# Kernel tuning notes

Hardware: AMD Instinct MI355X
Metric: run time of the kernel (lower is better)

Reference implementation:

```python
import jax, jax.numpy as jnp
import numpy as np

H = W = 32      # latent grid
WS = 8          # window size
NH = 8          # heads
C = 512         # channels
SHIFTS = (0, WS // 2)  # depth-2 Swin stage: W-MSA then SW-MSA


def _rel_pos_index(ws):
    coords = np.stack(np.meshgrid(np.arange(ws), np.arange(ws), indexing='ij'))
    flat = coords.reshape(2, -1)
    rel = (flat[:, :, None] - flat[:, None, :]).transpose(1, 2, 0).copy()
    rel[:, :, 0] += ws - 1
    rel[:, :, 1] += ws - 1
    rel[:, :, 0] *= 2 * ws - 1
    return jnp.asarray(rel.sum(-1))  # (ws*ws, ws*ws) int


def _attn_mask(h, w, ws, shift):
    img = np.zeros((h, w))
    cnt = 0
    sl = (slice(0, -ws), slice(-ws, -shift), slice(-shift, None))
    for hs in sl:
        for wsl in sl:
            img[hs, wsl] = cnt
            cnt += 1
    mw = img.reshape(h // ws, ws, w // ws, ws).transpose(0, 2, 1, 3).reshape(-1, ws * ws)
    m = mw[:, None, :] - mw[:, :, None]  # matches unsqueeze(1) - unsqueeze(2)
    return jnp.asarray(np.where(m != 0, -100.0, 0.0).astype(np.float32))  # (nW, N, N)


def _ln(x, g, b, eps=1e-5):
    mu = x.mean(-1, keepdims=True)
    var = ((x - mu) ** 2).mean(-1, keepdims=True)
    return (x - mu) * jax.lax.rsqrt(var + eps) * g + b


def _swin_block(x, shift, mask, rpi, n1g, n1b, qw, qb, rpb, pw, pb, n2g, n2b, f1w, f1b, f2w, f2b):
    B, L, Cc = x.shape
    N = WS * WS
    hd = Cc // NH
    shortcut = x
    h = _ln(x, n1g, n1b).reshape(B, H, W, Cc)
    if shift > 0:
        h = jnp.roll(h, (-shift, -shift), (1, 2))
    # window partition -> (B*nW, N, C)
    hw = h.reshape(B, H // WS, WS, W // WS, WS, Cc).transpose(0, 1, 3, 2, 4, 5).reshape(-1, N, Cc)
    qkv = (hw @ qw + qb).reshape(-1, N, 3, NH, hd).transpose(2, 0, 3, 1, 4)
    q, k, v = qkv[0], qkv[1], qkv[2]
    attn = jnp.einsum('bhnd,bhmd->bhnm', q * (hd ** -0.5), k)
    bias = rpb[rpi.reshape(-1)].reshape(N, N, NH).transpose(2, 0, 1)  # (NH, N, N)
    attn = attn + bias[None]
    if mask is not None:
        nW = mask.shape[0]
        attn = attn.reshape(-1, nW, NH, N, N) + mask[None, :, None]
        attn = attn.reshape(-1, NH, N, N)
    attn = jax.nn.softmax(attn, axis=-1)
    o = jnp.einsum('bhnm,bhmd->bhnd', attn, v).transpose(0, 2, 1, 3).reshape(-1, N, Cc)
    o = o @ pw + pb
    # window reverse
    o = o.reshape(B, H // WS, W // WS, WS, WS, Cc).transpose(0, 1, 3, 2, 4, 5).reshape(B, H, W, Cc)
    if shift > 0:
        o = jnp.roll(o, (shift, shift), (1, 2))
    x = shortcut + o.reshape(B, L, Cc)
    h2 = _ln(x, n2g, n2b)
    x = x + (jax.nn.gelu(h2 @ f1w + f1b, approximate=False) @ f2w + f2b)
    return x


def setup_inputs() -> dict:
    key = jax.random.key(0)
    ks = jax.random.split(key, 8)
    B, D, K = 32, 2, 4096
    s = 0.02
    return {
        'x': jax.random.normal(ks[0], (B, H * W, C), jnp.float32),
        'norm1_g': jnp.ones((D, C), jnp.float32),
        'norm1_b': jnp.zeros((D, C), jnp.float32),
        'qkv_w': jax.random.normal(ks[1], (D, C, 3 * C), jnp.float32) * s,
        'qkv_b': jnp.zeros((D, 3 * C), jnp.float32),
        'rpb_table': jax.random.normal(ks[2], (D, (2 * WS - 1) ** 2, NH), jnp.float32) * s,
        'proj_w': jax.random.normal(ks[3], (D, C, C), jnp.float32) * s,
        'proj_b': jnp.zeros((D, C), jnp.float32),
        'norm2_g': jnp.ones((D, C), jnp.float32),
        'norm2_b': jnp.zeros((D, C), jnp.float32),
        'fc1_w': jax.random.normal(ks[4], (D, C, 4 * C), jnp.float32) * s,
        'fc1_b': jnp.zeros((D, 4 * C), jnp.float32),
        'fc2_w': jax.random.normal(ks[5], (D, 4 * C, C), jnp.float32) * s,
        'fc2_b': jnp.zeros((D, C), jnp.float32),
        'codebook': jax.random.normal(ks[6], (K, C), jnp.float32),
    }


def reference(x, norm1_g, norm1_b, qkv_w, qkv_b, rpb_table, proj_w, proj_b,
              norm2_g, norm2_b, fc1_w, fc1_b, fc2_w, fc2_b, codebook):
    B, L, Cc = x.shape
    rpi = _rel_pos_index(WS)
    masks = [None, _attn_mask(H, W, WS, SHIFTS[1])]
    for i, shift in enumerate(SHIFTS):
        x = _swin_block(x, shift, masks[i], rpi,
                        norm1_g[i], norm1_b[i], qkv_w[i], qkv_b[i], rpb_table[i],
                        proj_w[i], proj_b[i], norm2_g[i], norm2_b[i],
                        fc1_w[i], fc1_b[i], fc2_w[i], fc2_b[i])
    # nearest-neighbor codebook quantization (cdist + argmin + gather)
    flat = x.reshape(-1, Cc)
    d = ((flat ** 2).sum(-1, keepdims=True)
         - 2.0 * flat @ codebook.T
         + (codebook ** 2).sum(-1))  # (B*L, K)
    idx = jnp.argmin(d, axis=-1)
    quant = codebook[idx]
    # straight-through estimator
    quant = flat + jax.lax.stop_gradient(quant - flat)
    return quant.reshape(B, L, Cc), idx.reshape(B, L)
```

## Files before the change

kernel.cpp:

```cpp
#include <hip/hip_runtime.h>
#include <math.h>

#define DEV __device__ __forceinline__

typedef __attribute__((ext_vector_type(8))) _Float16 f16x8;
typedef __attribute__((ext_vector_type(8))) short short8;
typedef __attribute__((ext_vector_type(4))) float f32x4;

namespace {

constexpr int C = 512;
constexpr int ROWS = 32768;
constexpr float LSCALE = 2048.0f;
constexpr float LINV   = 1.0f / 2048.0f;
constexpr float F16MIN = 6.1035156e-5f;

DEV void f2hsplit(float x, short& hs, short& ls) {
  _Float16 h = (_Float16)x;
  float hf = (float)h;
  if (fabsf(hf) < F16MIN) { h = (_Float16)0.0f; hf = 0.f; }
  _Float16 l = (_Float16)((x - hf) * LSCALE);
  if (fabsf((float)l) < F16MIN) l = (_Float16)0.0f;
  hs = __builtin_bit_cast(short, h);
  ls = __builtin_bit_cast(short, l);
}

DEV unsigned umn(unsigned a, unsigned b) { return a < b ? a : b; }
DEV unsigned umx(unsigned a, unsigned b) { return a > b ? a : b; }

DEV unsigned packkey(float d, int col) {
  unsigned u = __builtin_bit_cast(unsigned, d);
  u = (u & 0x80000000u) ? ~u : (u | 0x80000000u);
  return (u & 0xFFFFF000u) | (unsigned)col;
}
DEV float unpackd(unsigned k) {
  unsigned u = (k & 0x80000000u) ? (k ^ 0x80000000u) : ~k;
  return __builtin_bit_cast(float, u);
}

DEV int rowmap(int r, int shift) {
  int b  = r >> 10;
  int w  = (r >> 6) & 15;
  int wy = w >> 2, wx = w & 3;
  int ii = r & 63;
  int iy = ii >> 3, ix = ii & 7;
  int y = (wy * 8 + iy + shift) & 31;
  int x = (wx * 8 + ix + shift) & 31;
  return (b << 10) + (y << 5) + x;
}

DEV int region(int y) { return (y < 24) ? 0 : ((y < 28) ? 1 : 2); }

typedef __attribute__((address_space(1))) const unsigned int gu32;
typedef __attribute__((address_space(3))) unsigned int lu32;
DEV void gload16(const void* g, void* l) {
  __builtin_amdgcn_global_load_lds((gu32*)g, (lu32*)l, 16, 0, 0);
}

__global__ __launch_bounds__(256) void ln_split_kernel(
    const float* __restrict__ src, short* __restrict__ Hp, short* __restrict__ Lp,
    const float* __restrict__ g, const float* __restrict__ b,
    int shift, int windowed) {
  int wid  = (blockIdx.x * 256 + threadIdx.x) >> 6;
  int lane = threadIdx.x & 63;
  if (wid >= ROWS) return;
  int srcRow = windowed ? rowmap(wid, shift) : wid;
  const float* s = src + (size_t)srcRow * C + lane * 8;
  float v[8];
  *(float4*)(v)     = *(const float4*)(s);
  *(float4*)(v + 4) = *(const float4*)(s + 4);
  float sum = 0.f;
#pragma unroll
  for (int j = 0; j < 8; j++) sum += v[j];
#pragma unroll
  for (int o = 32; o >= 1; o >>= 1) sum += __shfl_xor(sum, o);
  float mu = sum * (1.0f / 512.0f);
  float vs = 0.f;
#pragma unroll
  for (int j = 0; j < 8; j++) { float d = v[j] - mu; vs += d * d; }
#pragma unroll
  for (int o = 32; o >= 1; o >>= 1) vs += __shfl_xor(vs, o);
  float rs = rsqrtf(vs * (1.0f / 512.0f) + 1e-5f);
  float gg[8], bb[8];
  *(float4*)gg       = *(const float4*)&g[lane * 8];
  *(float4*)(gg + 4) = *(const float4*)&g[lane * 8 + 4];
  *(float4*)bb       = *(const float4*)&b[lane * 8];
  *(float4*)(bb + 4) = *(const float4*)&b[lane * 8 + 4];
  short8 hv, lv;
#pragma unroll
  for (int j = 0; j < 8; j++) {
    float o8 = (v[j] - mu) * rs * gg[j] + bb[j];
    short hh, ll;
    f2hsplit(o8, hh, ll);
    hv[j] = hh; lv[j] = ll;
  }
  *(short8*)&Hp[(size_t)wid * C + lane * 8] = hv;
  *(short8*)&Lp[(size_t)wid * C + lane * 8] = lv;
}

__global__ __launch_bounds__(256) void rowss_kernel(
    const float* __restrict__ src, float* __restrict__ dst, int nrows) {
  int wid  = (blockIdx.x * 256 + threadIdx.x) >> 6;
  int lane = threadIdx.x & 63;
  if (wid >= nrows) return;
  const float* s = src + (size_t)wid * C + lane * 8;
  float4 a  = *(const float4*)s;
  float4 b4 = *(const float4*)(s + 4);
  float sum = a.x*a.x + a.y*a.y + a.z*a.z + a.w*a.w
            + b4.x*b4.x + b4.y*b4.y + b4.z*b4.z + b4.w*b4.w;
#pragma unroll
  for (int o = 32; o >= 1; o >>= 1) sum += __shfl_xor(sum, o);
  if (lane == 0) dst[wid] = sum;
}

__global__ __launch_bounds__(256) void wconvT_kernel(
    const float* __restrict__ W, short* __restrict__ Hp, short* __restrict__ Lp,
    int K, int N) {
  __shared__ float t[32][33];
  int tx = threadIdx.x, ty = threadIdx.y;
  int n0 = blockIdx.x * 32, k0 = blockIdx.y * 32;
#pragma unroll
  for (int r = 0; r < 4; r++) {
    int k = ty + r * 8;
    t[k][tx] = W[(size_t)(k0 + k) * N + n0 + tx];
  }
  __syncthreads();
#pragma unroll
  for (int r = 0; r < 4; r++) {
    int n = ty + r * 8;
    short h, l;
    f2hsplit(t[tx][n], h, l);
    Hp[(size_t)(n0 + n) * K + k0 + tx] = h;
    Lp[(size_t)(n0 + n) * K + k0 + tx] = l;
  }
}

__global__ __launch_bounds__(256) void wconv_kernel(
    const float* __restrict__ W, short* __restrict__ Hp, short* __restrict__ Lp) {
  size_t i = ((size_t)blockIdx.x * 256 + threadIdx.x) * 4;
  float4 a = *(const float4*)&W[i];
  float v[4] = {a.x, a.y, a.z, a.w};
  short hv[4], lv[4];
#pragma unroll
  for (int j = 0; j < 4; j++) f2hsplit(v[j], hv[j], lv[j]);
  *(short4*)&Hp[i] = *(short4*)hv;
  *(short4*)&Lp[i] = *(short4*)lv;
}

template <int EPI>
__global__ __launch_bounds__(512) void mgemm(
    const short* __restrict__ Ah, const short* __restrict__ Al,
    const short* __restrict__ Bh, const short* __restrict__ Bl,
    const int K, const float* __restrict__ bias,
    float* __restrict__ outF, short* __restrict__ outH, short* __restrict__ outL,
    const int ldo,
    const float* __restrict__ resid, const int rowOff, const int perm, const int shift) {
  __shared__ short lds[16384];
  const int m0 = blockIdx.x * 128, n0 = blockIdx.y * 128;
  const int t  = threadIdx.x;
  const int wv = t >> 6, ln = t & 63;
  const int wr = (wv >> 2) * 64, wc = (wv & 3) * 32;
  const int l15 = ln & 15, l4 = ln >> 4;

  f32x4 accH[4][2], accL[4][2];
#pragma unroll
  for (int mf = 0; mf < 4; mf++)
#pragma unroll
    for (int nf = 0; nf < 2; nf++) {
      accH[mf][nf] = (f32x4){0.f, 0.f, 0.f, 0.f};
      accL[mf][nf] = (f32x4){0.f, 0.f, 0.f, 0.f};
    }

  const int srow = ln >> 2;
  const int scol = ((ln & 3) ^ ((ln >> 3) & 3)) * 8;

  short* As_h = lds;
  short* Bs_h = lds + 4096;
  short* As_l = lds + 8192;
  short* Bs_l = lds + 12288;

  auto frag = [&](const short* lt, int rbase) -> f16x8 {
    int r = rbase + l15;
    int kc = l4 ^ ((r >> 1) & 3);
    return *(const f16x8*)(lt + (r >> 4) * 512 + (r & 15) * 32 + kc * 8);
  };

  for (int k0 = 0; k0 < K; k0 += 32) {
    size_t ra = (size_t)(m0 + wv * 16 + srow) * K + k0 + scol;
    size_t rb = (size_t)(n0 + wv * 16 + srow) * K + k0 + scol;
    gload16(Ah + ra, As_h + wv * 512);
    gload16(Bh + rb, Bs_h + wv * 512);
    gload16(Al + ra, As_l + wv * 512);
    gload16(Bl + rb, Bs_l + wv * 512);
    __syncthreads();
    f16x8 ah[4], bh[2], bl[2];
#pragma unroll
    for (int mf = 0; mf < 4; mf++) ah[mf] = frag(As_h, wr + mf * 16);
#pragma unroll
    for (int nf = 0; nf < 2; nf++) bh[nf] = frag(Bs_h, wc + nf * 16);
#pragma unroll
    for (int mf = 0; mf < 4; mf++)
#pragma unroll
      for (int nf = 0; nf < 2; nf++)
        accH[mf][nf] = __builtin_amdgcn_mfma_f32_16x16x32_f16(ah[mf], bh[nf], accH[mf][nf], 0, 0, 0);
#pragma unroll
    for (int nf = 0; nf < 2; nf++) bl[nf] = frag(Bs_l, wc + nf * 16);
#pragma unroll
    for (int mf = 0; mf < 4; mf++)
#pragma unroll
      for (int nf = 0; nf < 2; nf++)
        accL[mf][nf] = __builtin_amdgcn_mfma_f32_16x16x32_f16(ah[mf], bl[nf], accL[mf][nf], 0, 0, 0);
#pragma unroll
    for (int mf = 0; mf < 4; mf++) {
      f16x8 al = frag(As_l, wr + mf * 16);
#pragma unroll
      for (int nf = 0; nf < 2; nf++)
        accL[mf][nf] = __builtin_amdgcn_mfma_f32_16x16x32_f16(al, bh[nf], accL[mf][nf], 0, 0, 0);
    }
    __syncthreads();
  }

  f32x4 acc[4][2];
#pragma unroll
  for (int mf = 0; mf < 4; mf++)
#pragma unroll
    for (int nf = 0; nf < 2; nf++)
#pragma unroll
      for (int r = 0; r < 4; r++)
        acc[mf][nf][r] = fmaf(accL[mf][nf][r], LINV, accH[mf][nf][r]);

  if (EPI == 0) {
#pragma unroll
    for (int mf = 0; mf < 4; mf++)
#pragma unroll
      for (int r = 0; r < 4; r++) {
        int row = m0 + wr + mf * 16 + l4 * 4 + r;
        float* op = outF + (size_t)row * ldo;
#pragma unroll
        for (int nf = 0; nf < 2; nf++) {
          int col = n0 + wc + nf * 16 + l15;
          op[col] = acc[mf][nf][r] + bias[col];
        }
      }
  } else if (EPI == 1) {
#pragma unroll
    for (int mf = 0; mf < 4; mf++)
#pragma unroll
      for (int r = 0; r < 4; r++) {
        int row = m0 + wr + mf * 16 + l4 * 4 + r;
#pragma unroll
        for (int nf = 0; nf < 2; nf++) {
          int col = n0 + wc + nf * 16 + l15;
          float v = acc[mf][nf][r] + bias[col];
          v = 0.5f * v * (1.0f + erff(v * 0.70710678118654752f));
          short h, l;
          f2hsplit(v, h, l);
          outH[(size_t)row * ldo + col] = h;
          outL[(size_t)row * ldo + col] = l;
        }
      }
  } else {
#pragma unroll
    for (int mf = 0; mf < 4; mf++)
#pragma unroll
      for (int r = 0; r < 4; r++) {
        int row = m0 + wr + mf * 16 + l4 * 4 + r;
        int orow = perm ? rowmap(row, shift) : (row + rowOff);
        const float* rp = resid + (size_t)orow * ldo;
        float* op = outF + (size_t)orow * ldo;
#pragma unroll
        for (int nf = 0; nf < 2; nf++) {
          int col = n0 + wc + nf * 16 + l15;
          float v = rp[col] + acc[mf][nf][r] + bias[col];
          op[col] = v;
          if (EPI == 4) {
            short h, l;
            f2hsplit(v, h, l);
            outH[(size_t)orow * ldo + col] = h;
            outL[(size_t)orow * ldo + col] = l;
          }
        }
      }
  }
}

__global__ __launch_bounds__(256) void vqgemm(
    const short* __restrict__ Ah, const short* __restrict__ Bh,
    const float* __restrict__ c2, unsigned* __restrict__ pk) {
  __shared__ short lds[16384];
  const int bid = blockIdx.x;
  const int xcd = bid & 7, idx = bid >> 3;
  const int m0 = (xcd * 32 + (idx & 31)) * 128;
  const int ny = idx >> 5;
  const int n0 = ny * 128;
  const int K = 512;
  const int t  = threadIdx.x;
  const int wv = t >> 6, ln = t & 63;
  const int wr = (wv >> 1) * 64, wc = (wv & 1) * 64;
  const int l15 = ln & 15, l4 = ln >> 4;

  f32x4 acc[4][4];
#pragma unroll
  for (int mf = 0; mf < 4; mf++)
#pragma unroll
    for (int nf = 0; nf < 4; nf++) acc[mf][nf] = (f32x4){0.f, 0.f, 0.f, 0.f};

  const int srow = ln >> 2;
  const int scol = ((ln & 3) ^ ((ln >> 3) & 3)) * 8;

  short* As = lds;
  short* Bs = lds + 8192;

  auto frag = [&](const short* lt, int rbase) -> f16x8 {
    int r = rbase + l15;
    int kc = l4 ^ ((r >> 1) & 3);
    return *(const f16x8*)(lt + (r >> 4) * 512 + (r & 15) * 32 + kc * 8);
  };

  for (int k0 = 0; k0 < K; k0 += 64) {
#pragma unroll
    for (int q = 0; q < 8; q++) {
      int s = wv * 8 + q;
      int c = s & 15;
      int base0 = (s < 16) ? m0 : n0;
      const short* src = (s < 16) ? Ah : Bh;
      short* dst = ((s < 16) ? As : Bs) + c * 512;
      size_t ga = (size_t)(base0 + (c & 7) * 16 + srow) * K + k0 + (c >> 3) * 32 + scol;
      gload16(src + ga, dst);
    }
    __syncthreads();
#pragma unroll
    for (int kh = 0; kh < 2; kh++) {
      const short* Ab = As + kh * 4096;
      const short* Bb = Bs + kh * 4096;
      f16x8 ah[4], bh[4];
#pragma unroll
      for (int mf = 0; mf < 4; mf++) ah[mf] = frag(Ab, wr + mf * 16);
#pragma unroll
      for (int nf = 0; nf < 4; nf++) bh[nf] = frag(Bb, wc + nf * 16);
#pragma unroll
      for (int mf = 0; mf < 4; mf++)
#pragma unroll
        for (int nf = 0; nf < 4; nf++)
          acc[mf][nf] = __builtin_amdgcn_mfma_f32_16x16x32_f16(ah[mf], bh[nf], acc[mf][nf], 0, 0, 0);
    }
    __syncthreads();
  }

  unsigned* hk = (unsigned*)(void*)lds;
#pragma unroll
  for (int mf = 0; mf < 4; mf++)
#pragma unroll
    for (int r = 0; r < 4; r++) {
      int wrow = wr + mf * 16 + l4 * 4 + r;
      unsigned k1 = 0xFFFFFFFFu, k2 = 0xFFFFFFFFu;
#pragma unroll
      for (int nf = 0; nf < 4; nf++) {
        int col = n0 + wc + nf * 16 + l15;
        float d = c2[col] - 2.0f * acc[mf][nf][r];
        unsigned kk = packkey(d, col);
        if (kk < k1) { k2 = k1; k1 = kk; }
        else if (kk < k2) { k2 = kk; }
      }
#pragma unroll
      for (int o = 1; o <= 8; o <<= 1) {
        unsigned b1 = (unsigned)__shfl_xor((int)k1, o);
        unsigned b2 = (unsigned)__shfl_xor((int)k2, o);
        unsigned m1 = umn(k1, b1);
        unsigned m2 = umn(umx(k1, b1), umn(k2, b2));
        k1 = m1; k2 = m2;
      }
      if (l15 == 0) {
        hk[wrow * 4 + (wv & 1) * 2 + 0] = k1;
        hk[wrow * 4 + (wv & 1) * 2 + 1] = k2;
      }
    }
  __syncthreads();
  if (t < 128) {
    unsigned a1 = hk[t * 4 + 0], a2 = hk[t * 4 + 1];
    unsigned b1 = hk[t * 4 + 2], b2 = hk[t * 4 + 3];
    unsigned m1 = umn(a1, b1);
    unsigned m2 = umn(umx(a1, b1), umn(a2, b2));
    size_t base = (size_t)(m0 + t) * 64 + ny * 2;
    pk[base + 0] = m1;
    pk[base + 1] = m2;
  }
}

__global__ __launch_bounds__(256) void vq_out_kernel(
    const unsigned* __restrict__ pk, const float* __restrict__ x,
    const float* __restrict__ cb,
    float* __restrict__ outq, float* __restrict__ outidx) {
  int r = blockIdx.x * 4 + (threadIdx.x >> 6);
  int lane = threadIdx.x & 63;
  unsigned key = pk[(size_t)r * 64 + lane];
  unsigned kmin = key;
#pragma unroll
  for (int o = 32; o >= 1; o >>= 1) kmin = umn(kmin, (unsigned)__shfl_xor((int)kmin, o));
  float dmin = unpackd(kmin);
  unsigned long long mask = __ballot(unpackd(key) <= dmin + 2.0f);

  const float* xr = x + (size_t)r * C + lane * 8;
  float4 xa = *(const float4*)xr;
  float4 xb = *(const float4*)(xr + 4);

  float bestd = 3.4e38f;
  int   besti = 0x7fffffff;
  while (mask) {
    int l = __ffsll(mask) - 1;
    mask &= mask - 1;
    int col = ((unsigned)__shfl((int)key, l)) & 0xFFFu;
    const float* cr = cb + (size_t)col * C + lane * 8;
    float4 ca = *(const float4*)cr;
    float4 cb4 = *(const float4*)(cr + 4);
    float s = 0.f;
    s = fmaf(ca.x, ca.x - 2.f * xa.x, s);
    s = fmaf(ca.y, ca.y - 2.f * xa.y, s);
    s = fmaf(ca.z, ca.z - 2.f * xa.z, s);
    s = fmaf(ca.w, ca.w - 2.f * xa.w, s);
    s = fmaf(cb4.x, cb4.x - 2.f * xb.x, s);
    s = fmaf(cb4.y, cb4.y - 2.f * xb.y, s);
    s = fmaf(cb4.z, cb4.z - 2.f * xb.z, s);
    s = fmaf(cb4.w, cb4.w - 2.f * xb.w, s);
#pragma unroll
    for (int o = 32; o >= 1; o >>= 1) s += __shfl_xor(s, o);
    if (s < bestd || (s == bestd && col < besti)) { bestd = s; besti = col; }
  }
  const float4* src = (const float4*)(cb + (size_t)besti * C + lane * 8);
  float4*       dst = (float4*)(outq + (size_t)r * C + lane * 8);
  dst[0] = src[0];
  dst[1] = src[1];
  if (lane == 0) outidx[r] = (float)besti;
}

__global__ __launch_bounds__(256) void attn_kernel(
    const float* __restrict__ qkv,
    const float* __restrict__ rpb,
    short* __restrict__ Hout, short* __restrict__ Lout,
    int winOff, int shift) {
  int wl = blockIdx.x;
  int h  = blockIdx.y;
  int t  = threadIdx.x;
  __shared__ float q[64][64], k[64][64], v[64][64], pT[64][64];

  const float* base = qkv + (size_t)wl * 64 * 1536 + h * 64;
#pragma unroll
  for (int rep = 0; rep < 4; rep++) {
    int f = t + rep * 256;
    int i = f >> 4, dq = (f & 15) * 4;
    const float* rowp = base + (size_t)i * 1536 + dq;
    float4 qv = *(const float4*)(rowp);
    float4 kv = *(const float4*)(rowp + 512);
    float4 vv = *(const float4*)(rowp + 1024);
    q[i][dq] = qv.x * 0.125f; q[i][dq + 1] = qv.y * 0.125f;
    q[i][dq + 2] = qv.z * 0.125f; q[i][dq + 3] = qv.w * 0.125f;
    *(float4*)&k[i][dq] = kv;
    *(float4*)&v[i][dq] = vv;
  }
  __syncthreads();

  int i  = t >> 2;
  int jg = t & 3;
  int wim = (winOff + wl) & 15;
  int wy = wim >> 2, wx = wim & 3;
  int iy = i >> 3, ix = i & 7;

  float qreg[64];
#pragma unroll
  for (int d = 0; d < 64; d += 4) *(float4*)&qreg[d] = *(float4*)&q[i][d];

  int ci = 0;
  if (shift) ci = region(wy * 8 + iy) * 3 + region(wx * 8 + ix);

  float sc[16];
#pragma unroll
  for (int jj = 0; jj < 16; jj++) {
    int j = jg * 16 + jj;
    float s = 0.f;
#pragma unroll
    for (int d = 0; d < 64; d += 4) {
      float4 kv = *(float4*)&k[j][d];
      s = fmaf(qreg[d], kv.x, s);
      s = fmaf(qreg[d + 1], kv.y, s);
      s = fmaf(qreg[d + 2], kv.z, s);
      s = fmaf(qreg[d + 3], kv.w, s);
    }
    int jy = j >> 3, jx = j & 7;
    s += rpb[((iy - jy + 7) * 15 + (ix - jx + 7)) * 8 + h];
    if (shift) {
      int cj = region(wy * 8 + jy) * 3 + region(wx * 8 + jx);
      if (ci != cj) s -= 100.0f;
    }
    sc[jj] = s;
  }
  float mx = sc[0];
#pragma unroll
  for (int jj = 1; jj < 16; jj++) mx = fmaxf(mx, sc[jj]);
  mx = fmaxf(mx, __shfl_xor(mx, 1));
  mx = fmaxf(mx, __shfl_xor(mx, 2));
  float sum = 0.f;
#pragma unroll
  for (int jj = 0; jj < 16; jj++) { sc[jj] = expf(sc[jj] - mx); sum += sc[jj]; }
  sum += __shfl_xor(sum, 1);
  sum += __shfl_xor(sum, 2);
  float inv = 1.0f / sum;
#pragma unroll
  for (int jj = 0; jj < 16; jj++) pT[jg * 16 + jj][i] = sc[jj] * inv;
  __syncthreads();

  float accv[16];
#pragma unroll
  for (int dd = 0; dd < 16; dd++) accv[dd] = 0.f;
  for (int j = 0; j < 64; j++) {
    float pij = pT[j][i];
#pragma unroll
    for (int dd = 0; dd < 16; dd += 4) {
      float4 vv = *(float4*)&v[j][jg * 16 + dd];
      accv[dd]     = fmaf(pij, vv.x, accv[dd]);
      accv[dd + 1] = fmaf(pij, vv.y, accv[dd + 1]);
      accv[dd + 2] = fmaf(pij, vv.z, accv[dd + 2]);
      accv[dd + 3] = fmaf(pij, vv.w, accv[dd + 3]);
    }
  }
  size_t obase = ((size_t)(winOff + wl) * 64 + i) * 512 + h * 64 + jg * 16;
  short8 hv, lv;
#pragma unroll
  for (int half = 0; half < 2; half++) {
#pragma unroll
    for (int j = 0; j < 8; j++) {
      short hh, ll;
      f2hsplit(accv[half * 8 + j], hh, ll);
      hv[j] = hh; lv[j] = ll;
    }
    *(short8*)&Hout[obase + half * 8] = hv;
    *(short8*)&Lout[obase + half * 8] = lv;
  }
}

}

extern "C" void kernel_launch(void* const* d_in, const int* in_sizes, int n_in,
                              void* d_out, int out_size, void* d_ws, size_t ws_size,
                              hipStream_t stream) {
  const float* x_in = (const float*)d_in[0];
  const float* n1g  = (const float*)d_in[1];
  const float* n1b  = (const float*)d_in[2];
  const float* qkvw = (const float*)d_in[3];
  const float* qkvb = (const float*)d_in[4];
  const float* rpb  = (const float*)d_in[5];
  const float* pw   = (const float*)d_in[6];
  const float* pb   = (const float*)d_in[7];
  const float* n2g  = (const float*)d_in[8];
  const float* n2b  = (const float*)d_in[9];
  const float* f1w  = (const float*)d_in[10];
  const float* f1b  = (const float*)d_in[11];
  const float* f2w  = (const float*)d_in[12];
  const float* f2b_ = (const float*)d_in[13];
  const float* cb   = (const float*)d_in[14];

  float* outq   = (float*)d_out;
  float* outidx = outq + 16777216;
  short* Hbuf = (short*)d_out;
  short* Lbuf = Hbuf + (size_t)ROWS * 512;

  char* ws = (char*)d_ws;
  float* Abuf = (float*)ws;
  short* Wb   = (short*)(ws + ((size_t)64 << 20));
  char*  Cbuf = ws + ((size_t)96 << 20);
  const int Rrows = (ws_size >= ((size_t)232 << 20)) ? 16384
                  : (ws_size >= ((size_t)160 << 20)) ? 8192
                  : (ws_size >= ((size_t)128 << 20)) ? 4096 : 2048;

  const int SZ_QKV = 512 * 1536, SZ_P = 512 * 512, SZ_F1 = 512 * 2048, SZ_F2 = 2048 * 512;
  const int PB = (SZ_QKV + SZ_P + SZ_F1 + SZ_F2) * 2;
  short* cbH = Wb + (size_t)2 * PB;
  short* cbL = cbH + 4096 * 512;

  for (int blk = 0; blk < 2; blk++) {
    short* base = Wb + (size_t)blk * PB;
    short* qH = base;          short* qL = qH + SZ_QKV;
    short* pH = qL + SZ_QKV;   short* pL = pH + SZ_P;
    short* f1H = pL + SZ_P;    short* f1L = f1H + SZ_F1;
    short* f2H = f1L + SZ_F1;  short* f2L = f2H + SZ_F2;
    wconvT_kernel<<<dim3(48, 16), dim3(32, 8), 0, stream>>>(qkvw + (size_t)blk * SZ_QKV, qH, qL, 512, 1536);
    wconvT_kernel<<<dim3(16, 16), dim3(32, 8), 0, stream>>>(pw + (size_t)blk * SZ_P, pH, pL, 512, 512);
    wconvT_kernel<<<dim3(64, 16), dim3(32, 8), 0, stream>>>(f1w + (size_t)blk * SZ_F1, f1H, f1L, 512, 2048);
    wconvT_kernel<<<dim3(16, 64), dim3(32, 8), 0, stream>>>(f2w + (size_t)blk * SZ_F2, f2H, f2L, 2048, 512);
  }
  wconv_kernel<<<2048, 256, 0, stream>>>(cb, cbH, cbL);

  const int nch = ROWS / Rrows;
  for (int blk = 0; blk < 2; blk++) {
    short* base = Wb + (size_t)blk * PB;
    short* qH = base;          short* qL = qH + SZ_QKV;
    short* pH = qL + SZ_QKV;   short* pL = pH + SZ_P;
    short* f1H = pL + SZ_P;    short* f1L = f1H + SZ_F1;
    short* f2H = f1L + SZ_F1;  short* f2L = f2H + SZ_F2;
    const float* xcur = blk ? (const float*)Abuf : x_in;
    int shift = blk ? 4 : 0;

    ln_split_kernel<<<8192, 256, 0, stream>>>(xcur, Hbuf, Lbuf, n1g + blk * 512, n1b + blk * 512, shift, 1);

    float* Cq = (float*)Cbuf;
    for (int ch = 0; ch < nch; ch++) {
      int r0 = ch * Rrows;
      mgemm<0><<<dim3(Rrows / 128, 12), 512, 0, stream>>>(
          Hbuf + (size_t)r0 * 512, Lbuf + (size_t)r0 * 512, qH, qL, 512,
          qkvb + blk * 1536, Cq, nullptr, nullptr, 1536,
          nullptr, 0, 0, 0);
      attn_kernel<<<dim3(Rrows / 64, 8), 256, 0, stream>>>(
          Cq, rpb + blk * 1800, Hbuf, Lbuf, r0 >> 6, shift);
    }

    mgemm<2><<<dim3(256, 4), 512, 0, stream>>>(
        Hbuf, Lbuf, pH, pL, 512, pb + blk * 512,
        Abuf, nullptr, nullptr, 512,
        blk ? (const float*)Abuf : x_in, 0, 1, shift);

    ln_split_kernel<<<8192, 256, 0, stream>>>(Abuf, Hbuf, Lbuf, n2g + blk * 512, n2b + blk * 512, 0, 0);

    short* gh = (short*)Cbuf;
    short* gl = gh + (size_t)Rrows * 2048;
    for (int ch = 0; ch < nch; ch++) {
      int r0 = ch * Rrows;
      mgemm<1><<<dim3(Rrows / 128, 16), 512, 0, stream>>>(
          Hbuf + (size_t)r0 * 512, Lbuf + (size_t)r0 * 512, f1H, f1L, 512,
          f1b + blk * 2048, nullptr, gh, gl, 2048,
          nullptr, 0, 0, 0);
      if (blk == 0) {
        mgemm<2><<<dim3(Rrows / 128, 4), 512, 0, stream>>>(
            gh, gl, f2H, f2L, 2048, f2b_ + blk * 512,
            Abuf, nullptr, nullptr, 512,
            Abuf, r0, 0, 0);
      } else {
        mgemm<4><<<dim3(Rrows / 128, 4), 512, 0, stream>>>(
            gh, gl, f2H, f2L, 2048, f2b_ + blk * 512,
            Abuf, Hbuf, Lbuf, 512,
            Abuf, r0, 0, 0);
      }
    }
  }

  float*    c2  = (float*)Cbuf;
  unsigned* pkb = (unsigned*)(Cbuf + ((size_t)64 << 10));
  rowss_kernel<<<1024, 256, 0, stream>>>(cb, c2, 4096);
  vqgemm<<<8192, 256, 0, stream>>>(Hbuf, cbH, c2, pkb);
  vq_out_kernel<<<8192, 256, 0, stream>>>(pkb, Abuf, cb, outq, outidx);
}
```

Measured before the change: 2.424 ms.

## Double-buffer LDS in split-f16 GEMM and restructure VQ GEMM to 512 threads

The mgemm kernel now keeps two LDS buffers and issues the global-to-LDS loads for the next K slice before computing the current one, so memory latency can overlap with MFMA work. This doubles its shared-memory footprint and may lower occupancy. The vqgemm kernel moves to 512 threads with 8 waves, each computing a 64x32 sub-tile. It steps K by 32 with the same double-buffered staging, and its top-2 reduction now merges four partial results per row instead of two.

```diff
diff --git a/kernel.cpp b/kernel.cpp
--- a/kernel.cpp
+++ b/kernel.cpp
@@ -155,7 +155,7 @@
     float* __restrict__ outF, short* __restrict__ outH, short* __restrict__ outL,
     const int ldo,
     const float* __restrict__ resid, const int rowOff, const int perm, const int shift) {
-  __shared__ short lds[16384];
+  __shared__ short lds[32768];
   const int m0 = blockIdx.x * 128, n0 = blockIdx.y * 128;
   const int t  = threadIdx.x;
   const int wv = t >> 6, ln = t & 63;
@@ -174,25 +174,31 @@
   const int srow = ln >> 2;
   const int scol = ((ln & 3) ^ ((ln >> 3) & 3)) * 8;
 
-  short* As_h = lds;
-  short* Bs_h = lds + 4096;
-  short* As_l = lds + 8192;
-  short* Bs_l = lds + 12288;
-
+  auto stage = [&](int buf, int k0) {
+    short* b = lds + buf * 16384;
+    size_t ra = (size_t)(m0 + wv * 16 + srow) * K + k0 + scol;
+    size_t rb = (size_t)(n0 + wv * 16 + srow) * K + k0 + scol;
+    gload16(Ah + ra, b + wv * 512);
+    gload16(Bh + rb, b + 4096 + wv * 512);
+    gload16(Al + ra, b + 8192 + wv * 512);
+    gload16(Bl + rb, b + 12288 + wv * 512);
+  };
   auto frag = [&](const short* lt, int rbase) -> f16x8 {
     int r = rbase + l15;
     int kc = l4 ^ ((r >> 1) & 3);
     return *(const f16x8*)(lt + (r >> 4) * 512 + (r & 15) * 32 + kc * 8);
   };
 
+  stage(0, 0);
+  __syncthreads();
+  int cur = 0;
   for (int k0 = 0; k0 < K; k0 += 32) {
-    size_t ra = (size_t)(m0 + wv * 16 + srow) * K + k0 + scol;
-    size_t rb = (size_t)(n0 + wv * 16 + srow) * K + k0 + scol;
-    gload16(Ah + ra, As_h + wv * 512);
-    gload16(Bh + rb, Bs_h + wv * 512);
-    gload16(Al + ra, As_l + wv * 512);
-    gload16(Bl + rb, Bs_l + wv * 512);
-    __syncthreads();
+    if (k0 + 32 < K) stage(cur ^ 1, k0 + 32);
+    const short* base = lds + cur * 16384;
+    const short* As_h = base;
+    const short* Bs_h = base + 4096;
+    const short* As_l = base + 8192;
+    const short* Bs_l = base + 12288;
     f16x8 ah[4], bh[2], bl[2];
 #pragma unroll
     for (int mf = 0; mf < 4; mf++) ah[mf] = frag(As_h, wr + mf * 16);
@@ -218,6 +224,7 @@
         accL[mf][nf] = __builtin_amdgcn_mfma_f32_16x16x32_f16(al, bh[nf], accL[mf][nf], 0, 0, 0);
     }
     __syncthreads();
+    cur ^= 1;
   }
 
   f32x4 acc[4][2];
@@ -284,7 +291,7 @@
   }
 }
 
-__global__ __launch_bounds__(256) void vqgemm(
+__global__ __launch_bounds__(512) void vqgemm(
     const short* __restrict__ Ah, const short* __restrict__ Bh,
     const float* __restrict__ c2, unsigned* __restrict__ pk) {
   __shared__ short lds[16384];
@@ -296,55 +303,49 @@
   const int K = 512;
   const int t  = threadIdx.x;
   const int wv = t >> 6, ln = t & 63;
-  const int wr = (wv >> 1) * 64, wc = (wv & 1) * 64;
+  const int wr = (wv >> 2) * 64, wc = (wv & 3) * 32;
   const int l15 = ln & 15, l4 = ln >> 4;
 
-  f32x4 acc[4][4];
+  f32x4 acc[4][2];
 #pragma unroll
   for (int mf = 0; mf < 4; mf++)
 #pragma unroll
-    for (int nf = 0; nf < 4; nf++) acc[mf][nf] = (f32x4){0.f, 0.f, 0.f, 0.f};
+    for (int nf = 0; nf < 2; nf++) acc[mf][nf] = (f32x4){0.f, 0.f, 0.f, 0.f};
 
   const int srow = ln >> 2;
   const int scol = ((ln & 3) ^ ((ln >> 3) & 3)) * 8;
 
-  short* As = lds;
-  short* Bs = lds + 8192;
-
+  auto stage = [&](int buf, int k0) {
+    short* b = lds + buf * 8192;
+    size_t ra = (size_t)(m0 + wv * 16 + srow) * K + k0 + scol;
+    size_t rb = (size_t)(n0 + wv * 16 + srow) * K + k0 + scol;
+    gload16(Ah + ra, b + wv * 512);
+    gload16(Bh + rb, b + 4096 + wv * 512);
+  };
   auto frag = [&](const short* lt, int rbase) -> f16x8 {
     int r = rbase + l15;
     int kc = l4 ^ ((r >> 1) & 3);
     return *(const f16x8*)(lt + (r >> 4) * 512 + (r & 15) * 32 + kc * 8);
   };
 
-  for (int k0 = 0; k0 < K; k0 += 64) {
-#pragma unroll
-    for (int q = 0; q < 8; q++) {
-      int s = wv * 8 + q;
-      int c = s & 15;
-      int base0 = (s < 16) ? m0 : n0;
-      const short* src = (s < 16) ? Ah : Bh;
-      short* dst = ((s < 16) ? As : Bs) + c * 512;
-      size_t ga = (size_t)(base0 + (c & 7) * 16 + srow) * K + k0 + (c >> 3) * 32 + scol;
-      gload16(src + ga, dst);
-    }
+  stage(0, 0);
+  __syncthreads();
+  int cur = 0;
+  for (int k0 = 0; k0 < K; k0 += 32) {
+    if (k0 + 32 < K) stage(cur ^ 1, k0 + 32);
+    const short* base = lds + cur * 8192;
+    f16x8 ah[4], bh[2];
+#pragma unroll
+    for (int mf = 0; mf < 4; mf++) ah[mf] = frag(base, wr + mf * 16);
+#pragma unroll
+    for (int nf = 0; nf < 2; nf++) bh[nf] = frag(base + 4096, wc + nf * 16);
+#pragma unroll
+    for (int mf = 0; mf < 4; mf++)
+#pragma unroll
+      for (int nf = 0; nf < 2; nf++)
+        acc[mf][nf] = __builtin_amdgcn_mfma_f32_16x16x32_f16(ah[mf], bh[nf], acc[mf][nf], 0, 0, 0);
     __syncthreads();
-#pragma unroll
-    for (int kh = 0; kh < 2; kh++) {
-      const short* Ab = As + kh * 4096;
-      const short* Bb = Bs + kh * 4096;
-      f16x8 ah[4], bh[4];
-#pragma unroll
-      for (int mf = 0; mf < 4; mf++) ah[mf] = frag(Ab, wr + mf * 16);
-#pragma unroll
-      for (int nf = 0; nf < 4; nf++) bh[nf] = frag(Bb, wc + nf * 16);
-#pragma unroll
-      for (int mf = 0; mf < 4; mf++)
-#pragma unroll
-        for (int nf = 0; nf < 4; nf++)
-          acc[mf][nf] = __builtin_amdgcn_mfma_f32_16x16x32_f16(ah[mf], bh[nf], acc[mf][nf], 0, 0, 0);
-    }
-    __syncthreads();
+    cur ^= 1;
   }
 
   unsigned* hk = (unsigned*)(void*)lds;
@@ -355,7 +356,7 @@
       int wrow = wr + mf * 16 + l4 * 4 + r;
       unsigned k1 = 0xFFFFFFFFu, k2 = 0xFFFFFFFFu;
 #pragma unroll
-      for (int nf = 0; nf < 4; nf++) {
+      for (int nf = 0; nf < 2; nf++) {
         int col = n0 + wc + nf * 16 + l15;
         float d = c2[col] - 2.0f * acc[mf][nf][r];
         unsigned kk = packkey(d, col);
@@ -371,14 +372,22 @@
         k1 = m1; k2 = m2;
       }
       if (l15 == 0) {
-        hk[wrow * 4 + (wv & 1) * 2 + 0] = k1;
-        hk[wrow * 4 + (wv & 1) * 2 + 1] = k2;
+        hk[wrow * 8 + (wv & 3) * 2 + 0] = k1;
+        hk[wrow * 8 + (wv & 3) * 2 + 1] = k2;
       }
     }
   __syncthreads();
   if (t < 128) {
-    unsigned a1 = hk[t * 4 + 0], a2 = hk[t * 4 + 1];
-    unsigned b1 = hk[t * 4 + 2], b2 = hk[t * 4 + 3];
+    unsigned q1[4], q2[4];
+#pragma unroll
+    for (int i = 0; i < 4; i++) {
+      q1[i] = hk[t * 8 + i * 2];
+      q2[i] = hk[t * 8 + i * 2 + 1];
+    }
+    unsigned a1 = umn(q1[0], q1[1]);
+    unsigned a2 = umn(umx(q1[0], q1[1]), umn(q2[0], q2[1]));
+    unsigned b1 = umn(q1[2], q1[3]);
+    unsigned b2 = umn(umx(q1[2], q1[3]), umn(q2[2], q2[3]));
     unsigned m1 = umn(a1, b1);
     unsigned m2 = umn(umx(a1, b1), umn(a2, b2));
     size_t base = (size_t)(m0 + t) * 64 + ny * 2;
@@ -644,6 +653,6 @@
   float*    c2  = (float*)Cbuf;
   unsigned* pkb = (unsigned*)(Cbuf + ((size_t)64 << 10));
   rowss_kernel<<<1024, 256, 0, stream>>>(cb, c2, 4096);
-  vqgemm<<<8192, 256, 0, stream>>>(Hbuf, cbH, c2, pkb);
+  vqgemm<<<8192, 512, 0, stream>>>(Hbuf, cbH, c2, pkb);
   vq_out_kernel<<<8192, 256, 0, stream>>>(pkb, Abuf, cb, outq, outidx);
 }
```

Result: faster. 2.343 ms (-3.4%).
